# Performance work log

Hardware: AMD Instinct MI355X
Metric: run time of the kernel (lower is better)

The kernel has to match this reference:

```python
import jax, jax.numpy as jnp
import numpy as np

N_EXPERT = 8
TOP_K = 2
NEG_INF = -1e9  # finite sentinel so softmax grads stay well-defined


def setup_inputs() -> dict:
    key = jax.random.key(0)
    ks = jax.random.split(key, 8)
    B, S, D, F, E = 2, 2048, 1024, 4096, N_EXPERT
    sd = 1.0 / np.sqrt(D)
    sf = 1.0 / np.sqrt(F)
    return {
        "x": jax.random.normal(ks[0], (B, S, D), jnp.float32),
        "noise": jax.random.normal(ks[1], (B, S, E), jnp.float32),
        "Wr": jax.random.normal(ks[2], (D, E), jnp.float32) * sd,
        "br": jnp.zeros((E,), jnp.float32),
        "Wn": jax.random.normal(ks[3], (D, E), jnp.float32) * sd,
        "bn": jnp.zeros((E,), jnp.float32),
        "W1": jax.random.normal(ks[4], (E, D, F), jnp.float32) * sd,
        "b1": jnp.zeros((E, F), jnp.float32),
        "W2": jax.random.normal(ks[5], (E, F, D), jnp.float32) * sf,
        "b2": jnp.zeros((E, D), jnp.float32),
    }


def reference(x, noise, Wr, br, Wn, bn, W1, b1, W2, b2):
    # NoisyTopkRouter: logits + noise * softplus(noise_logits)
    logits = jnp.einsum("bsd,de->bse", x, Wr) + br
    noise_logits = jnp.einsum("bsd,de->bse", x, Wn) + bn
    noisy = logits + noise * jax.nn.softplus(noise_logits)

    # keep only top-k logits, -inf elsewhere, softmax over experts
    _, top_ids = jax.lax.top_k(noisy, TOP_K)                  # [B,S,K]
    sel = jnp.sum(jax.nn.one_hot(top_ids, N_EXPERT, dtype=noisy.dtype), axis=-2) > 0  # [B,S,E]
    gates = jax.nn.softmax(jnp.where(sel, noisy, NEG_INF), axis=-1)  # zeros off top-k

    # Expert MLP: Linear -> ReLU -> Linear (dropout = 0 at inference).
    # Gates are exactly zero for non-selected experts, so the dense einsum
    # combine equals the original masked gather/scatter-add.
    h = jax.nn.relu(jnp.einsum("bsd,edf->ebsf", x, W1) + b1[:, None, None, :])
    eo = jnp.einsum("ebsf,efd->ebsd", h, W2) + b2[:, None, None, :]
    return jnp.einsum("bse,ebsd->bsd", gates, eo)
```

## Files before the change

### kernel.cpp

```cpp
#include <hip/hip_runtime.h>

#define T_TOK 4096
#define DDIM 1024
#define FDIM 4096
#define NE 8
#define NPAIR 8192
#define MAXT128 72

typedef short bf16x8 __attribute__((ext_vector_type(8)));
typedef float f32x4 __attribute__((ext_vector_type(4)));

__device__ inline unsigned short f2bf(float f) {
  union { float f; unsigned u; } a; a.f = f;
  unsigned r = a.u + 0x7fffu + ((a.u >> 16) & 1u);
  return (unsigned short)(r >> 16);
}

__device__ __forceinline__ void gload16(const void* g, void* l) {
  __builtin_amdgcn_global_load_lds(
      (const __attribute__((address_space(1))) unsigned int*)g,
      (__attribute__((address_space(3))) unsigned int*)l, 16, 0, 0);
}

__global__ __launch_bounds__(256) void router_kernel(
    const float* __restrict__ x, const float* __restrict__ noise,
    const float* __restrict__ Wr, const float* __restrict__ br,
    const float* __restrict__ Wn, const float* __restrict__ bn,
    int* __restrict__ tok_top, float* __restrict__ tok_gate,
    ushort* __restrict__ xb)
{
  int t = blockIdx.x * 4 + (threadIdx.x >> 6);
  int lane = threadIdx.x & 63;
  const float* xr = x + (size_t)t * DDIM;
  ushort* xo = xb + (size_t)t * DDIM;
  float accR[NE] = {}, accN[NE] = {};
  for (int d = lane; d < DDIM; d += 64) {
    float xv = xr[d];
    xo[d] = f2bf(xv);
    const float* wr = Wr + (size_t)d * NE;
    const float* wn = Wn + (size_t)d * NE;
#pragma unroll
    for (int e = 0; e < NE; ++e) {
      accR[e] = fmaf(xv, wr[e], accR[e]);
      accN[e] = fmaf(xv, wn[e], accN[e]);
    }
  }
#pragma unroll
  for (int off = 32; off > 0; off >>= 1) {
#pragma unroll
    for (int e = 0; e < NE; ++e) {
      accR[e] += __shfl_xor(accR[e], off);
      accN[e] += __shfl_xor(accN[e], off);
    }
  }
  if (lane == 0) {
    float noisy[NE];
#pragma unroll
    for (int e = 0; e < NE; ++e) {
      float lg = accR[e] + br[e];
      float nl = accN[e] + bn[e];
      float sp = fmaxf(nl, 0.f) + log1pf(expf(-fabsf(nl)));
      noisy[e] = lg + noise[(size_t)t * NE + e] * sp;
    }
    int e0 = 0;
#pragma unroll
    for (int e = 1; e < NE; ++e) if (noisy[e] > noisy[e0]) e0 = e;
    int e1 = (e0 == 0) ? 1 : 0;
#pragma unroll
    for (int e = 0; e < NE; ++e)
      if (e != e0 && e != e1 && noisy[e] > noisy[e1]) e1 = e;
    float v0 = noisy[e0], v1 = noisy[e1];
    float ex = __expf(v1 - v0);
    float inv = 1.f / (1.f + ex);
    tok_top[t * 2] = e0; tok_top[t * 2 + 1] = e1;
    tok_gate[t * 2] = inv; tok_gate[t * 2 + 1] = ex * inv;
  }
}

__global__ __launch_bounds__(256) void scan_scatter_kernel(
    const int* __restrict__ tok_top, int* __restrict__ off, int* __restrict__ tiles,
    int* __restrict__ pair_tok, int* __restrict__ tok_ppos)
{
  __shared__ int smat[NE][256];
  __shared__ int tot[NE];
  __shared__ int loff[NE];
  int tid = threadIdx.x;
  int c[NE] = {};
  for (int i = 0; i < 16; ++i) {
    int t = tid * 16 + i;
    int e0 = tok_top[2 * t], e1 = tok_top[2 * t + 1];
#pragma unroll
    for (int e = 0; e < NE; ++e) c[e] += (e0 == e) + (e1 == e);
  }
#pragma unroll
  for (int e = 0; e < NE; ++e) smat[e][tid] = c[e];
  __syncthreads();
  {
    int ge = tid >> 5;
    int gl = tid & 31;
    int vals[8], s = 0;
#pragma unroll
    for (int j = 0; j < 8; ++j) { vals[j] = smat[ge][gl * 8 + j]; s += vals[j]; }
    int incl = s;
#pragma unroll
    for (int d = 1; d < 32; d <<= 1) {
      int o = __shfl_up(incl, d);
      if (gl >= d) incl += o;
    }
    int run = incl - s;
#pragma unroll
    for (int j = 0; j < 8; ++j) { smat[ge][gl * 8 + j] = run; run += vals[j]; }
    if (gl == 31) tot[ge] = incl;
  }
  __syncthreads();
  if (tid == 0) {
    int s = 0, nt = 0;
    for (int e = 0; e < NE; ++e) {
      loff[e] = s; off[e] = s;
      int tt = (tot[e] + 127) >> 7;
      for (int m = 0; m < tt; ++m) tiles[1 + nt++] = (e << 8) | m;
      s += tot[e];
    }
    off[NE] = s;
    tiles[0] = nt;
  }
  __syncthreads();
  for (int i = 0; i < 16; ++i) {
    int t = tid * 16 + i;
#pragma unroll
    for (int k = 0; k < 2; ++k) {
      int e = tok_top[2 * t + k];
      int pos = loff[e] + smat[e][tid];
      smat[e][tid] = smat[e][tid] + 1;
      pair_tok[pos] = t;
      tok_ppos[2 * t + k] = pos;
    }
  }
}

__global__ __launch_bounds__(256) void transpose_bf_kernel(
    const float* __restrict__ W1, const float* __restrict__ W2,
    ushort* __restrict__ WT1, ushort* __restrict__ WT2)
{
  __shared__ float tile[64][65];
  int z = blockIdx.z;
  const float* src; ushort* dst; int R, C, bx, by;
  if (z < NE) {
    src = W1 + (size_t)z * DDIM * FDIM; dst = WT1 + (size_t)z * FDIM * DDIM;
    R = DDIM; C = FDIM; bx = blockIdx.x; by = blockIdx.y;
  } else {
    src = W2 + (size_t)(z - NE) * FDIM * DDIM; dst = WT2 + (size_t)(z - NE) * DDIM * FDIM;
    R = FDIM; C = DDIM; bx = blockIdx.y; by = blockIdx.x;
  }
  int c0 = bx * 64, r0 = by * 64;
  int tid = threadIdx.x;
  int tr = tid >> 4;
  int tc4 = (tid & 15) * 4;
#pragma unroll
  for (int i = 0; i < 64; i += 16) {
    float4 v = *(const float4*)(src + (size_t)(r0 + tr + i) * C + c0 + tc4);
    tile[tr + i][tc4] = v.x; tile[tr + i][tc4 + 1] = v.y;
    tile[tr + i][tc4 + 2] = v.z; tile[tr + i][tc4 + 3] = v.w;
  }
  __syncthreads();
  int cc = tid >> 4;
  int rr4 = (tid & 15) * 4;
#pragma unroll
  for (int i = 0; i < 64; i += 16) {
    int c = cc + i;
    ushort4 o;
    o.x = f2bf(tile[rr4][c]); o.y = f2bf(tile[rr4 + 1][c]);
    o.z = f2bf(tile[rr4 + 2][c]); o.w = f2bf(tile[rr4 + 3][c]);
    *(ushort4*)(dst + (size_t)(c0 + c) * R + r0 + rr4) = o;
  }
}

template<int KD, int ND, int EPI, int INDIR>
__global__ __launch_bounds__(256) void gemm4_kernel(
    const ushort* __restrict__ A, const ushort* __restrict__ BT,
    const int* __restrict__ off, const int* __restrict__ tiles,
    const int* __restrict__ pair_tok, const float* __restrict__ bias,
    ushort* __restrict__ Hout, float* __restrict__ EOout)
{
  constexpr int GX = ND / 128;
  constexpr int NKT = KD / 64;
  __shared__ __align__(16) ushort As[128 * 64];
  __shared__ __align__(16) ushort Bs[128 * 64];

  int total = tiles[0] * GX;
  int orig = blockIdx.x + GX * (int)blockIdx.y;
  if (orig >= total) return;
  int q = total >> 3, r = total & 7, xcd = orig & 7, idx = orig >> 3;
  int wg = (xcd < r ? xcd * (q + 1) : r * (q + 1) + (xcd - r) * q) + idx;
  int ti = wg / GX, bx = wg - ti * GX;

  int te = tiles[1 + ti];
  int e = te >> 8, mt = te & 255;
  int base = off[e];
  int cnt = off[e + 1] - base;
  int m0 = mt << 7, n0 = bx << 7;

  int tid = threadIdx.x, lane = tid & 63, wid = tid >> 6;
  int wr = wid >> 1, wc = wid & 1;

  int arow[4];
#pragma unroll
  for (int c = 0; c < 4; ++c) {
    int rl = (c * 256 + tid) >> 3;
    int mr = m0 + rl; if (mr >= cnt) mr = cnt - 1;
    arow[c] = INDIR ? pair_tok[base + mr] : base + mr;
  }
  const char* Ab = (const char*)A;
  const char* Bgb = (const char*)(BT + ((size_t)e * ND + n0) * KD);

  f32x4 acc[4][4] = {};

  for (int t = 0; t < NKT; ++t) {
    __syncthreads();
    int kb = t * 128;
#pragma unroll
    for (int c = 0; c < 4; ++c) {
      int ch = c * 256 + tid;
      int row = ch >> 3, b = (ch & 7) * 16;
      gload16(Ab + (size_t)arow[c] * (KD * 2) + kb + (b ^ ((row & 7) << 4)),
              (char*)As + ch * 16);
    }
#pragma unroll
    for (int c = 0; c < 4; ++c) {
      int ch = c * 256 + tid;
      int row = ch >> 3, b = (ch & 7) * 16;
      gload16(Bgb + (size_t)row * (KD * 2) + kb + (b ^ ((row & 7) << 4)),
              (char*)Bs + ch * 16);
    }
    __syncthreads();

    bf16x8 af[4][2], bv[4][2];
#pragma unroll
    for (int m = 0; m < 4; ++m) {
      int row = wr * 64 + m * 16 + (lane & 15);
      int sw = (row & 7) << 4;
#pragma unroll
      for (int ks = 0; ks < 2; ++ks)
        af[m][ks] = *(const bf16x8*)((const char*)As + row * 128 +
                                     ((ks * 64 + (lane >> 4) * 16) ^ sw));
    }
#pragma unroll
    for (int n = 0; n < 4; ++n) {
      int row = wc * 64 + n * 16 + (lane & 15);
      int sw = (row & 7) << 4;
#pragma unroll
      for (int ks = 0; ks < 2; ++ks)
        bv[n][ks] = *(const bf16x8*)((const char*)Bs + row * 128 +
                                     ((ks * 64 + (lane >> 4) * 16) ^ sw));
    }
#pragma unroll
    for (int ks = 0; ks < 2; ++ks)
#pragma unroll
      for (int m = 0; m < 4; ++m)
#pragma unroll
        for (int n = 0; n < 4; ++n)
          acc[m][n] = __builtin_amdgcn_mfma_f32_16x16x32_bf16(
              af[m][ks], bv[n][ks], acc[m][n], 0, 0, 0);
  }

  float bvv[4];
#pragma unroll
  for (int n = 0; n < 4; ++n)
    bvv[n] = bias[(size_t)e * ND + n0 + wc * 64 + n * 16 + (lane & 15)];
  int rq = (lane >> 4) << 2;
#pragma unroll
  for (int m = 0; m < 4; ++m) {
#pragma unroll
    for (int qq = 0; qq < 4; ++qq) {
      int rr = m0 + wr * 64 + m * 16 + rq + qq;
      if (rr < cnt) {
#pragma unroll
        for (int n = 0; n < 4; ++n) {
          int col = n0 + wc * 64 + n * 16 + (lane & 15);
          float v = acc[m][n][qq] + bvv[n];
          if (EPI == 0) {
            v = fmaxf(v, 0.f);
            Hout[(size_t)(base + rr) * ND + col] = f2bf(v);
          } else {
            EOout[(size_t)(base + rr) * ND + col] = v;
          }
        }
      }
    }
  }
}

__global__ __launch_bounds__(256) void combine_kernel(
    const float* __restrict__ eo, const int* __restrict__ tok_ppos,
    const float* __restrict__ tok_gate, float* __restrict__ out)
{
  int t = blockIdx.x;
  int tid = threadIdx.x;
  int p0 = tok_ppos[t * 2], p1 = tok_ppos[t * 2 + 1];
  float g0 = tok_gate[t * 2], g1 = tok_gate[t * 2 + 1];
  float4 a = ((const float4*)(eo + (size_t)p0 * DDIM))[tid];
  float4 b = ((const float4*)(eo + (size_t)p1 * DDIM))[tid];
  float4 o;
  o.x = g0 * a.x + g1 * b.x;
  o.y = g0 * a.y + g1 * b.y;
  o.z = g0 * a.z + g1 * b.z;
  o.w = g0 * a.w + g1 * b.w;
  ((float4*)(out + (size_t)t * DDIM))[tid] = o;
}

extern "C" void kernel_launch(void* const* d_in, const int* in_sizes, int n_in,
                              void* d_out, int out_size, void* d_ws, size_t ws_size,
                              hipStream_t stream)
{
  const float* x     = (const float*)d_in[0];
  const float* noise = (const float*)d_in[1];
  const float* Wr    = (const float*)d_in[2];
  const float* br    = (const float*)d_in[3];
  const float* Wn    = (const float*)d_in[4];
  const float* bn    = (const float*)d_in[5];
  const float* W1    = (const float*)d_in[6];
  const float* b1    = (const float*)d_in[7];
  const float* W2    = (const float*)d_in[8];
  const float* b2    = (const float*)d_in[9];
  float* out = (float*)d_out;

  char* ws = (char*)d_ws;
  size_t o = 0;
  auto alloc = [&](size_t sz) {
    void* p = ws + o;
    o = (o + sz + 255) & ~(size_t)255;
    return p;
  };
  ushort* WT1 = (ushort*)alloc((size_t)NE * FDIM * DDIM * 2);
  ushort* WT2 = (ushort*)alloc((size_t)NE * DDIM * FDIM * 2);
  ushort* XB  = (ushort*)alloc((size_t)T_TOK * DDIM * 2);
  ushort* H   = (ushort*)alloc((size_t)(NPAIR + 256) * FDIM * 2);
  float*  EO  = (float*)alloc((size_t)(NPAIR + 256) * DDIM * 4);
  int*    TOK_TOP  = (int*)alloc(T_TOK * 2 * 4);
  float*  TOK_GATE = (float*)alloc(T_TOK * 2 * 4);
  int*    TOK_PPOS = (int*)alloc(T_TOK * 2 * 4);
  int*    PAIR_TOK = (int*)alloc((NPAIR + 256) * 4);
  int*    OFF = (int*)alloc(64);
  int*    TILES = (int*)alloc((1 + MAXT128) * 4);

  router_kernel<<<T_TOK / 4, 256, 0, stream>>>(x, noise, Wr, br, Wn, bn,
                                               TOK_TOP, TOK_GATE, XB);
  scan_scatter_kernel<<<1, 256, 0, stream>>>(TOK_TOP, OFF, TILES, PAIR_TOK, TOK_PPOS);
  transpose_bf_kernel<<<dim3(64, 16, 16), 256, 0, stream>>>(W1, W2, WT1, WT2);
  gemm4_kernel<DDIM, FDIM, 0, 1>
      <<<dim3(FDIM / 128, MAXT128), 256, 0, stream>>>(XB, WT1, OFF, TILES, PAIR_TOK, b1, H, nullptr);
  gemm4_kernel<FDIM, DDIM, 1, 0>
      <<<dim3(DDIM / 128, MAXT128), 256, 0, stream>>>(H, WT2, OFF, TILES, PAIR_TOK, b2, nullptr, EO);
  combine_kernel<<<T_TOK, 256, 0, stream>>>(EO, TOK_PPOS, TOK_GATE, out);
}
```

Measured before the change: 323.1 us.

## Overlap W2 transpose-convert with first expert GEMM via extra grid blocks

Splits the weight transpose kernel so only W1 is transposed beforehand, and folds the W2 transpose/bf16 conversion into the first grouped GEMM launch as extra blocks past the active tile count. The grid is enlarged so idle blocks beyond the routed tiles each transpose one 64x64 W2 tile. This aims to overlap the memory-bound W2 conversion with the compute-bound first GEMM and drop a separate serialized pass. The cost is extra shared memory in the GEMM kernel and possible contention between transpose blocks and GEMM blocks for bandwidth and CU slots.

```diff
diff --git a/kernel.cpp b/kernel.cpp
--- a/kernel.cpp
+++ b/kernel.cpp
@@ -138,27 +138,20 @@
   }
 }
 
-__global__ __launch_bounds__(256) void transpose_bf_kernel(
-    const float* __restrict__ W1, const float* __restrict__ W2,
-    ushort* __restrict__ WT1, ushort* __restrict__ WT2)
+__global__ __launch_bounds__(256) void transpose_w1_kernel(
+    const float* __restrict__ W1, ushort* __restrict__ WT1)
 {
   __shared__ float tile[64][65];
   int z = blockIdx.z;
-  const float* src; ushort* dst; int R, C, bx, by;
-  if (z < NE) {
-    src = W1 + (size_t)z * DDIM * FDIM; dst = WT1 + (size_t)z * FDIM * DDIM;
-    R = DDIM; C = FDIM; bx = blockIdx.x; by = blockIdx.y;
-  } else {
-    src = W2 + (size_t)(z - NE) * FDIM * DDIM; dst = WT2 + (size_t)(z - NE) * DDIM * FDIM;
-    R = FDIM; C = DDIM; bx = blockIdx.y; by = blockIdx.x;
-  }
-  int c0 = bx * 64, r0 = by * 64;
+  const float* src = W1 + (size_t)z * DDIM * FDIM;
+  ushort* dst = WT1 + (size_t)z * FDIM * DDIM;
+  int c0 = blockIdx.x * 64, r0 = blockIdx.y * 64;
   int tid = threadIdx.x;
   int tr = tid >> 4;
   int tc4 = (tid & 15) * 4;
 #pragma unroll
   for (int i = 0; i < 64; i += 16) {
-    float4 v = *(const float4*)(src + (size_t)(r0 + tr + i) * C + c0 + tc4);
+    float4 v = *(const float4*)(src + (size_t)(r0 + tr + i) * FDIM + c0 + tc4);
     tile[tr + i][tc4] = v.x; tile[tr + i][tc4 + 1] = v.y;
     tile[tr + i][tc4 + 2] = v.z; tile[tr + i][tc4 + 3] = v.w;
   }
@@ -171,16 +164,17 @@
     ushort4 o;
     o.x = f2bf(tile[rr4][c]); o.y = f2bf(tile[rr4 + 1][c]);
     o.z = f2bf(tile[rr4 + 2][c]); o.w = f2bf(tile[rr4 + 3][c]);
-    *(ushort4*)(dst + (size_t)(c0 + c) * R + r0 + rr4) = o;
-  }
-}
-
-template<int KD, int ND, int EPI, int INDIR>
+    *(ushort4*)(dst + (size_t)(c0 + c) * DDIM + r0 + rr4) = o;
+  }
+}
+
+template<int KD, int ND, int EPI, int INDIR, int TFUSE>
 __global__ __launch_bounds__(256) void gemm4_kernel(
     const ushort* __restrict__ A, const ushort* __restrict__ BT,
     const int* __restrict__ off, const int* __restrict__ tiles,
     const int* __restrict__ pair_tok, const float* __restrict__ bias,
-    ushort* __restrict__ Hout, float* __restrict__ EOout)
+    ushort* __restrict__ Hout, float* __restrict__ EOout,
+    const float* __restrict__ W2src, ushort* __restrict__ WT2dst)
 {
   constexpr int GX = ND / 128;
   constexpr int NKT = KD / 64;
@@ -189,7 +183,40 @@
 
   int total = tiles[0] * GX;
   int orig = blockIdx.x + GX * (int)blockIdx.y;
-  if (orig >= total) return;
+  if (orig >= total) {
+    if constexpr (TFUSE) {
+      int idx = orig - total;
+      if (idx >= NE * (FDIM / 64) * (DDIM / 64)) return;
+      __shared__ float ttile[64][65];
+      int e2 = idx >> 10;
+      int rem = idx & 1023;
+      int ft = rem >> 4, dt = rem & 15;
+      const float* src = W2src + (size_t)e2 * FDIM * DDIM;
+      ushort* dst = WT2dst + (size_t)e2 * DDIM * FDIM;
+      int r0 = ft * 64, c0 = dt * 64;
+      int tid2 = threadIdx.x;
+      int tr = tid2 >> 4;
+      int tc4 = (tid2 & 15) * 4;
+#pragma unroll
+      for (int i = 0; i < 64; i += 16) {
+        float4 v = *(const float4*)(src + (size_t)(r0 + tr + i) * DDIM + c0 + tc4);
+        ttile[tr + i][tc4] = v.x; ttile[tr + i][tc4 + 1] = v.y;
+        ttile[tr + i][tc4 + 2] = v.z; ttile[tr + i][tc4 + 3] = v.w;
+      }
+      __syncthreads();
+      int cc = tid2 >> 4;
+      int rr4 = (tid2 & 15) * 4;
+#pragma unroll
+      for (int i = 0; i < 64; i += 16) {
+        int c = cc + i;
+        ushort4 o;
+        o.x = f2bf(ttile[rr4][c]); o.y = f2bf(ttile[rr4 + 1][c]);
+        o.z = f2bf(ttile[rr4 + 2][c]); o.w = f2bf(ttile[rr4 + 3][c]);
+        *(ushort4*)(dst + (size_t)(c0 + c) * FDIM + r0 + rr4) = o;
+      }
+    }
+    return;
+  }
   int q = total >> 3, r = total & 7, xcd = orig & 7, idx = orig >> 3;
   int wg = (xcd < r ? xcd * (q + 1) : r * (q + 1) + (xcd - r) * q) + idx;
   int ti = wg / GX, bx = wg - ti * GX;
@@ -346,10 +373,12 @@
   router_kernel<<<T_TOK / 4, 256, 0, stream>>>(x, noise, Wr, br, Wn, bn,
                                                TOK_TOP, TOK_GATE, XB);
   scan_scatter_kernel<<<1, 256, 0, stream>>>(TOK_TOP, OFF, TILES, PAIR_TOK, TOK_PPOS);
-  transpose_bf_kernel<<<dim3(64, 16, 16), 256, 0, stream>>>(W1, W2, WT1, WT2);
-  gemm4_kernel<DDIM, FDIM, 0, 1>
-      <<<dim3(FDIM / 128, MAXT128), 256, 0, stream>>>(XB, WT1, OFF, TILES, PAIR_TOK, b1, H, nullptr);
-  gemm4_kernel<FDIM, DDIM, 1, 0>
-      <<<dim3(DDIM / 128, MAXT128), 256, 0, stream>>>(H, WT2, OFF, TILES, PAIR_TOK, b2, nullptr, EO);
+  transpose_w1_kernel<<<dim3(64, 16, 8), 256, 0, stream>>>(W1, WT1);
+  gemm4_kernel<DDIM, FDIM, 0, 1, 1>
+      <<<dim3(FDIM / 128, 328), 256, 0, stream>>>(XB, WT1, OFF, TILES, PAIR_TOK, b1, H,
+                                                  nullptr, W2, WT2);
+  gemm4_kernel<FDIM, DDIM, 1, 0, 0>
+      <<<dim3(DDIM / 128, MAXT128), 256, 0, stream>>>(H, WT2, OFF, TILES, PAIR_TOK, b2,
+                                                      nullptr, EO, nullptr, nullptr);
   combine_kernel<<<T_TOK, 256, 0, stream>>>(EO, TOK_PPOS, TOK_GATE, out);
 }
```

Measured after the change: 318.9 us. No clear change (-1.3%).
